# Kernel optimization log

Measured on AMD Instinct MI355X. Metric: run time of the kernel, lower is better.

The kernel has to match this reference:

```python
import jax, jax.numpy as jnp
import numpy as np

DIM = 1024
HEADS = 16
HEAD_DIM = DIM // HEADS
HIDDEN = 4096  # mlp_ratio * dim
SCALE = HEAD_DIM ** -0.5
LN_EPS = 1e-5


def softmax_one(x):
    # softmax with +1 in the denominator (after max subtraction), per source
    m = jnp.max(x, axis=-1, keepdims=True)
    e = jnp.exp(x - m)
    return e / (1.0 + jnp.sum(e, axis=-1, keepdims=True))


def layer_norm(x, g, b):
    mu = jnp.mean(x, axis=-1, keepdims=True)
    var = jnp.mean(jnp.square(x - mu), axis=-1, keepdims=True)
    return (x - mu) * jax.lax.rsqrt(var + LN_EPS) * g + b


def setup_inputs() -> dict:
    key = jax.random.key(0)
    ks = jax.random.split(key, 12)
    B, C, N = 2, DIM, 2048
    x = jax.random.normal(ks[0], (B, C, N), dtype=jnp.float32)
    mask = jax.random.randint(ks[1], (B, HEADS, N), 0, 2, dtype=jnp.int32)
    s = 0.02
    return {
        'x': x,
        'mask': mask,
        'qkv_w': jax.random.normal(ks[2], (3 * DIM, DIM), jnp.float32) * s,
        'qkv_b': jnp.zeros((3 * DIM,), jnp.float32),
        'proj_w': jax.random.normal(ks[3], (DIM, DIM), jnp.float32) * s,
        'proj_b': jnp.zeros((DIM,), jnp.float32),
        'fc1_w': jax.random.normal(ks[4], (HIDDEN, DIM), jnp.float32) * s,
        'fc1_b': jnp.zeros((HIDDEN,), jnp.float32),
        'ln_g': jnp.ones((HIDDEN,), jnp.float32),
        'ln_b': jnp.zeros((HIDDEN,), jnp.float32),
        'fc2_w': jax.random.normal(ks[5], (DIM, HIDDEN), jnp.float32) * s,
        'fc2_b': jnp.zeros((DIM,), jnp.float32),
    }


def reference(x, mask, qkv_w, qkv_b, proj_w, proj_b, fc1_w, fc1_b, ln_g, ln_b, fc2_w, fc2_b):
    B, C, N = x.shape
    xt = jnp.swapaxes(x, 1, 2)  # (B, N, C)

    # ----- attention -----
    qkv = xt @ qkv_w.T + qkv_b                      # (B, N, 3C)
    qkv = qkv.reshape(B, N, 3, HEADS, HEAD_DIM)
    qkv = jnp.transpose(qkv, (2, 0, 3, 1, 4))       # (3, B, H, N, Dh)
    q, k, v = qkv[0], qkv[1], qkv[2]
    scores = jnp.einsum('bhnd,bhmd->bhnm', q * SCALE, k)  # (B, H, N, N)
    scores = jnp.where(mask[:, :, :, None] == 0, -1e9, scores)
    attn = softmax_one(scores)
    out = jnp.einsum('bhnm,bhmd->bhnd', attn, v)    # (B, H, N, Dh)
    # faithful to source: permute(0,3,1,2).reshape(B,N,C) -> scrambled merge
    out = jnp.transpose(out, (0, 3, 1, 2)).reshape(B, N, C)
    out = out @ proj_w.T + proj_b

    # faithful residual: attn_out + ls1(attn_out) with ls1 = Identity
    h = out + out                                   # (B, N, C)

    # ----- MLP (timm Mlp: fc1 -> GELU -> LayerNorm -> fc2) -----
    m = h @ fc1_w.T + fc1_b
    m = jax.nn.gelu(m, approximate=False)
    m = layer_norm(m, ln_g, ln_b)
    m = m @ fc2_w.T + fc2_b
    y = h + m                                       # (B, N, C)

    return jnp.swapaxes(y, 1, 2)                    # (B, C, N)
```

## Files before the change

kernel.cpp:

```cpp
#include <hip/hip_runtime.h>
#include <math.h>

#define DIMC   1024
#define NTOK   2048
#define BATCH  2
#define HEADS  16
#define HDIM   64
#define HIDDEN 4096
#define MROWS  (BATCH*NTOK)
#define QSZ    ((size_t)BATCH*HEADS*NTOK*HDIM)
#define QSC    0.18033688f

typedef unsigned short ushort_t;
typedef __attribute__((ext_vector_type(8))) short short8;
typedef __attribute__((ext_vector_type(4))) float f32x4;
typedef __attribute__((ext_vector_type(4))) unsigned short us4;

__device__ __forceinline__ ushort_t f2b(float f) {
  union { float f; unsigned int u; } cv; cv.f = f;
  unsigned int u = cv.u;
  unsigned int r = (u + 0x7fffu + ((u >> 16) & 1u)) >> 16;
  return (ushort_t)r;
}

__device__ __forceinline__ float b2f(ushort_t b) {
  union { unsigned int u; float f; } cv; cv.u = ((unsigned int)b) << 16;
  return cv.f;
}

__device__ __forceinline__ float fexp2(float x) {
#if __has_builtin(__builtin_amdgcn_exp2f)
  return __builtin_amdgcn_exp2f(x);
#else
  return exp2f(x);
#endif
}

__device__ __forceinline__ void gl_lds16(const void* g, void* l) {
  __builtin_amdgcn_global_load_lds(
      (const __attribute__((address_space(1))) void*)g,
      (__attribute__((address_space(3))) void*)l, 16, 0, 0);
}

__global__ __launch_bounds__(256) void k_pre(const float* __restrict__ x,
                                             const float* __restrict__ w0,
                                             const float* __restrict__ w1,
                                             const float* __restrict__ w2,
                                             const float* __restrict__ w3,
                                             ushort_t* __restrict__ xt,
                                             ushort_t* __restrict__ o0,
                                             ushort_t* __restrict__ o1,
                                             ushort_t* __restrict__ o2,
                                             ushort_t* __restrict__ o3) {
  __shared__ float t[32][33];
  int bid = blockIdx.x;
  if (bid < 4096) {
    int b   = bid >> 11;
    int rem = bid & 2047;
    int n0  = (rem & 63) * 32;
    int c0  = (rem >> 6) * 32;
    int tx = threadIdx.x & 31, ty = threadIdx.x >> 5;
#pragma unroll
    for (int l = 0; l < 4; l++)
      t[ty + l * 8][tx] = x[((size_t)(b * DIMC + c0 + ty + l * 8)) * NTOK + n0 + tx];
    __syncthreads();
#pragma unroll
    for (int l = 0; l < 4; l++)
      xt[((size_t)(b * NTOK + n0 + ty + l * 8)) * DIMC + c0 + tx] = f2b(t[tx][ty + l * 8]);
  } else {
    int cb = bid - 4096;
    const float* in; ushort_t* out; int base;
    if (cb < 3072)      { in = w0; out = o0; base = cb; }
    else if (cb < 4096) { in = w1; out = o1; base = cb - 3072; }
    else if (cb < 8192) { in = w2; out = o2; base = cb - 4096; }
    else                { in = w3; out = o3; base = cb - 8192; }
    int i = base * 256 + threadIdx.x;
    float4 v = ((const float4*)in)[i];
    us4 o; o.x = f2b(v.x); o.y = f2b(v.y); o.z = f2b(v.z); o.w = f2b(v.w);
    ((us4*)out)[i] = o;
  }
}

template <int EPI, int NTX8, int KSTRIDE, int KLEN, int XROW>
__global__ __launch_bounds__(256) void k_gemm_bf16(const ushort_t* __restrict__ A,
                                                   const ushort_t* __restrict__ W,
                                                   const float* __restrict__ bias,
                                                   void* __restrict__ outv) {
  __shared__ ushort_t As[2][128 * 32];
  __shared__ ushort_t Bs[2][128 * 32];
  const int tid = threadIdx.x;
  const int lane = tid & 63, wv = tid >> 6;
  const int bid = blockIdx.x, kz = blockIdx.y;
  const int xcd = bid & 7, t = bid >> 3;
  const int row0 = XROW ? (xcd * NTX8 + (t % NTX8)) * 128 : (t / NTX8) * 128;
  const int col0 = XROW ? (t / NTX8) * 128 : (xcd * NTX8 + (t % NTX8)) * 128;
  const int wrow0 = (wv >> 1) * 64, wcol0 = (wv & 1) * 64;
  const int lm = lane & 15, lq = lane >> 4;
  const int srow = wv * 32 + (lane >> 2);
  const int gch = (lane & 3) ^ ((lane >> 3) & 3);
  const int sw8 = (lq ^ ((lm >> 1) & 3)) * 8;

  const ushort_t* Ab = A + (size_t)(row0 + srow) * KSTRIDE + (size_t)kz * KLEN + gch * 8;
  const ushort_t* Wb = W + (size_t)(col0 + srow) * KSTRIDE + (size_t)kz * KLEN + gch * 8;
  const size_t rstep = (size_t)16 * KSTRIDE;

  f32x4 acc[4][4];
#pragma unroll
  for (int i = 0; i < 4; i++)
#pragma unroll
    for (int j = 0; j < 4; j++) acc[i][j] = (f32x4){0.f, 0.f, 0.f, 0.f};

#define STAGE(buf, k0) do {                                      \
    gl_lds16(Ab + (k0),         &As[buf][wv * 1024]);            \
    gl_lds16(Ab + rstep + (k0), &As[buf][wv * 1024 + 512]);      \
    gl_lds16(Wb + (k0),         &Bs[buf][wv * 1024]);            \
    gl_lds16(Wb + rstep + (k0), &Bs[buf][wv * 1024 + 512]);      \
  } while (0)

  auto compute = [&](int buf) {
    short8 af[4], bf[4];
#pragma unroll
    for (int mi = 0; mi < 4; mi++)
      af[mi] = *(const short8*)&As[buf][(wrow0 + mi * 16 + lm) * 32 + sw8];
#pragma unroll
    for (int ni = 0; ni < 4; ni++)
      bf[ni] = *(const short8*)&Bs[buf][(wcol0 + ni * 16 + lm) * 32 + sw8];
#pragma unroll
    for (int mi = 0; mi < 4; mi++)
#pragma unroll
      for (int ni = 0; ni < 4; ni++)
        acc[mi][ni] = __builtin_amdgcn_mfma_f32_16x16x32_bf16(af[mi], bf[ni], acc[mi][ni], 0, 0, 0);
  };

  constexpr int S = KLEN / 32;
  STAGE(0, 0);
#pragma unroll 1
  for (int kk = 0; kk < S; kk++) {
    __syncthreads();
    if (kk + 1 < S) STAGE((kk + 1) & 1, (kk + 1) * 32);
    compute(kk & 1);
  }
#undef STAGE

#pragma unroll
  for (int mi = 0; mi < 4; mi++) {
#pragma unroll
    for (int ni = 0; ni < 4; ni++) {
#pragma unroll
      for (int r = 0; r < 4; r++) {
        const int row = row0 + wrow0 + mi * 16 + lq * 4 + r;
        const int col = col0 + wcol0 + ni * 16 + lm;
        float v = acc[mi][ni][r];
        if (EPI != 4) v += bias[col];
        if (EPI == 0) {
          int which = col >> 10, rem = col & 1023, hh = rem >> 6, d = rem & 63;
          int bb = row >> 11, n = row & 2047;
          size_t bh = (size_t)(bb * HEADS + hh);
          ushort_t* o16 = (ushort_t*)outv;
          if (which == 0)
            o16[(bh * NTOK + n) * HDIM + d] = f2b(v * QSC);
          else if (which == 1)
            o16[QSZ + (bh * NTOK + n) * HDIM + d] = f2b(v);
          else
            o16[2 * QSZ + (bh * HDIM + d) * NTOK + n] = f2b(v);
        } else {
          ((ushort_t*)outv)[(size_t)kz * MROWS * DIMC + (size_t)row * DIMC + col] = f2b(v);
        }
      }
    }
  }
}

template <int EPI, int KSTRIDE, int NCT, int NB8>
__global__ __launch_bounds__(512, 2) void k_gemm256(const ushort_t* __restrict__ A,
                                                    const ushort_t* __restrict__ W,
                                                    const float* __restrict__ bias,
                                                    void* __restrict__ outv) {
  __shared__ ushort_t As[2][256 * 64];
  __shared__ ushort_t Bs[2][256 * 64];
  const int tid = threadIdx.x;
  const int lane = tid & 63, wid = tid >> 6;
  const int wr = wid >> 2, wc = wid & 3;
  const int lm = lane & 15, quad = lane >> 4;
  const int bid = blockIdx.x, kz = blockIdx.y;
  const int lin = (bid & 7) * NB8 + (bid >> 3);
  const int row0 = (lin / NCT) * 256, col0 = (lin % NCT) * 256;
  const int swz = lm & 7;

  const int gch = (tid & 7) ^ ((tid >> 3) & 7);
  const ushort_t* Ab = A + (size_t)(row0 + (tid >> 3)) * KSTRIDE + (size_t)kz * 1024 + gch * 8;
  const ushort_t* Wb = W + (size_t)(col0 + (tid >> 3)) * KSTRIDE + (size_t)kz * 1024 + gch * 8;
  const int dbase = wid * 512;

  auto stA = [&](int buf, int half, int kt) {
    const ushort_t* s = Ab + (size_t)(half * 128) * KSTRIDE + kt * 64;
    gl_lds16(s,                &As[buf][half * 8192 + dbase]);
    gl_lds16(s + 64 * KSTRIDE, &As[buf][half * 8192 + 4096 + dbase]);
  };
  auto stB = [&](int buf, int half, int kt) {
    const ushort_t* s = Wb + (size_t)(half * 128) * KSTRIDE + kt * 64;
    gl_lds16(s,                &Bs[buf][half * 8192 + dbase]);
    gl_lds16(s + 64 * KSTRIDE, &Bs[buf][half * 8192 + 4096 + dbase]);
  };

  f32x4 acc[8][4];
#pragma unroll
  for (int i = 0; i < 8; i++)
#pragma unroll
    for (int j = 0; j < 4; j++) acc[i][j] = (f32x4){0.f, 0.f, 0.f, 0.f};

  short8 af[4][2], bf[4][2];

  auto rdAf = [&](int buf, int mih) {
#pragma unroll
    for (int mi = 0; mi < 4; mi++)
#pragma unroll
      for (int ks = 0; ks < 2; ks++)
        af[mi][ks] = *(const short8*)&As[buf][(wr * 128 + (mih * 4 + mi) * 16 + lm) * 64 +
                                             (((ks * 4 + quad) ^ swz) * 8)];
  };
  auto rdBf = [&](int buf, int nh) {
#pragma unroll
    for (int nn = 0; nn < 2; nn++)
#pragma unroll
      for (int ks = 0; ks < 2; ks++)
        bf[nh * 2 + nn][ks] = *(const short8*)&Bs[buf][(wc * 64 + (nh * 2 + nn) * 16 + lm) * 64 +
                                                       (((ks * 4 + quad) ^ swz) * 8)];
  };
  auto quadMM = [&](int m0, int n0) {
    __builtin_amdgcn_s_setprio(1);
#pragma unroll
    for (int mi = 0; mi < 4; mi++)
#pragma unroll
      for (int ni = 0; ni < 2; ni++)
#pragma unroll
        for (int ks = 0; ks < 2; ks++)
          acc[m0 + mi][n0 + ni] = __builtin_amdgcn_mfma_f32_16x16x32_bf16(
              af[mi][ks], bf[n0 + ni][ks], acc[m0 + mi][n0 + ni], 0, 0, 0);
    __builtin_amdgcn_s_setprio(0);
  };

  constexpr int NT = 16;
  stB(0, 0, 0); stB(0, 1, 0);
  stA(0, 0, 0); stA(0, 1, 0);
  stB(1, 0, 1); stB(1, 1, 1);

#pragma unroll 1
  for (int kt = 0; kt < NT; kt++) {
    const int buf = kt & 1;
    if (kt + 1 < NT) __builtin_amdgcn_s_waitcnt(0x0F74);
    else             __builtin_amdgcn_s_waitcnt(0x0F70);
    __builtin_amdgcn_s_barrier();
    asm volatile("" ::: "memory");

    rdAf(buf, 0);
    rdBf(buf, 0);
    if (kt + 1 < NT) stA(buf ^ 1, 0, kt + 1);
    asm volatile("" ::: "memory");
    __builtin_amdgcn_s_barrier();
    quadMM(0, 0);
    __builtin_amdgcn_s_barrier();
    asm volatile("" ::: "memory");

    rdBf(buf, 1);
    if (kt + 1 < NT) stA(buf ^ 1, 1, kt + 1);
    asm volatile("" ::: "memory");
    __builtin_amdgcn_s_barrier();
    quadMM(0, 2);
    __builtin_amdgcn_s_barrier();
    asm volatile("" ::: "memory");

    rdAf(buf, 1);
    if (kt + 2 < NT) stB(buf, 0, kt + 2);
    asm volatile("" ::: "memory");
    __builtin_amdgcn_s_barrier();
    quadMM(4, 2);
    __builtin_amdgcn_s_barrier();
    asm volatile("" ::: "memory");

    if (kt + 2 < NT) stB(buf, 1, kt + 2);
    asm volatile("" ::: "memory");
    __builtin_amdgcn_s_barrier();
    quadMM(4, 0);
  }

#pragma unroll
  for (int mi = 0; mi < 8; mi++)
#pragma unroll
    for (int ni = 0; ni < 4; ni++)
#pragma unroll
      for (int r = 0; r < 4; r++) {
        const int row = row0 + wr * 128 + mi * 16 + quad * 4 + r;
        const int col = col0 + wc * 64 + ni * 16 + lm;
        if (EPI == 2) {
          ((ushort_t*)outv)[(size_t)row * HIDDEN + col] = f2b(acc[mi][ni][r] + bias[col]);
        } else {
          ((ushort_t*)outv)[(size_t)kz * MROWS * DIMC + (size_t)row * DIMC + col] = f2b(acc[mi][ni][r]);
        }
      }
}

__global__ __launch_bounds__(256) void k_comb_proj(const ushort_t* __restrict__ p0,
                                                   const ushort_t* __restrict__ p1,
                                                   const float* __restrict__ bias,
                                                   ushort_t* __restrict__ hb) {
  int i = blockIdx.x * 256 + threadIdx.x;
  int colb = (i & 255) * 4;
  us4 a = ((const us4*)p0)[i];
  us4 b = ((const us4*)p1)[i];
  us4 o;
  o.x = f2b(2.f * (b2f(a.x) + b2f(b.x) + bias[colb + 0]));
  o.y = f2b(2.f * (b2f(a.y) + b2f(b.y) + bias[colb + 1]));
  o.z = f2b(2.f * (b2f(a.z) + b2f(b.z) + bias[colb + 2]));
  o.w = f2b(2.f * (b2f(a.w) + b2f(b.w) + bias[colb + 3]));
  ((us4*)hb)[i] = o;
}

__global__ __launch_bounds__(256) void k_comb_fc2(const ushort_t* __restrict__ p,
                                                  const ushort_t* __restrict__ hb,
                                                  const float* __restrict__ bias,
                                                  float* __restrict__ out) {
  __shared__ float t[32][33];
  const size_t SL = (size_t)MROWS * DIMC;
  int b  = blockIdx.z;
  int c0 = blockIdx.y * 32, n0 = blockIdx.x * 32;
  int tx = threadIdx.x, ty = threadIdx.y;
#pragma unroll
  for (int l = 0; l < 4; l++) {
    size_t idx = ((size_t)(b * NTOK + n0 + ty + l * 8)) * DIMC + c0 + tx;
    t[ty + l * 8][tx] = b2f(p[idx]) + b2f(p[idx + SL]) + b2f(p[idx + 2 * SL]) +
                        b2f(p[idx + 3 * SL]) + b2f(hb[idx]) + bias[c0 + tx];
  }
  __syncthreads();
#pragma unroll
  for (int l = 0; l < 4; l++)
    out[((size_t)(b * DIMC + c0 + ty + l * 8)) * NTOK + n0 + tx] = t[tx][ty + l * 8];
}

__global__ __launch_bounds__(256) void k_attn_mfma(const ushort_t* __restrict__ qkv,
                                                   const int* __restrict__ mask,
                                                   ushort_t* __restrict__ scram) {
  __shared__ ushort_t Kl[2][64 * 64];
  __shared__ ushort_t Vl[2][64 * 64];
  __shared__ ushort_t Pl[4 * 32 * 72];
  const int tid = threadIdx.x;
  const int lane = tid & 63, w = tid >> 6;
  const int lm = lane & 15, quad = lane >> 4;
  const int bh = blockIdx.y, b = bh >> 4, h = bh & 15;
  const int q0 = blockIdx.x * 128 + w * 32;
  const ushort_t* qg  = qkv + (size_t)bh * NTOK * HDIM;
  const ushort_t* kg  = qkv + QSZ + (size_t)bh * NTOK * HDIM;
  const ushort_t* vTg = qkv + 2 * QSZ + (size_t)bh * HDIM * NTOK;
  ushort_t* Pw = &Pl[w * 32 * 72];

  const short8 ones = {0x3F80, 0x3F80, 0x3F80, 0x3F80, 0x3F80, 0x3F80, 0x3F80, 0x3F80};

  short8 qf[2][2];
#pragma unroll
  for (int qs = 0; qs < 2; qs++)
#pragma unroll
    for (int hf = 0; hf < 2; hf++)
      qf[qs][hf] = *(const short8*)&qg[(size_t)(q0 + qs * 16 + lm) * HDIM + hf * 32 + quad * 8];

  bool mk[2][4];
#pragma unroll
  for (int qs = 0; qs < 2; qs++)
#pragma unroll
    for (int r = 0; r < 4; r++)
      mk[qs][r] = mask[(size_t)bh * NTOK + q0 + qs * 16 + quad * 4 + r] != 0;

  f32x4 O[2][4], La[2];
#pragma unroll
  for (int qs = 0; qs < 2; qs++) {
    La[qs] = (f32x4){0.f, 0.f, 0.f, 0.f};
#pragma unroll
    for (int r = 0; r < 4; r++) O[qs][r] = (f32x4){0.f, 0.f, 0.f, 0.f};
  }

  const int s0 = tid, s1 = tid + 256;
  const int r0 = s0 >> 3, g0 = (s0 & 7) ^ (r0 & 7);
  const int r1 = s1 >> 3, g1 = (s1 & 7) ^ (r1 & 7);

  gl_lds16(kg + (size_t)r0 * HDIM + g0 * 8, &Kl[0][s0 * 8]);
  gl_lds16(kg + (size_t)r1 * HDIM + g1 * 8, &Kl[0][s1 * 8]);
  gl_lds16(vTg + (size_t)r0 * NTOK + g0 * 8, &Vl[0][s0 * 8]);
  gl_lds16(vTg + (size_t)r1 * NTOK + g1 * 8, &Vl[0][s1 * 8]);

  for (int kt = 0; kt < NTOK; kt += 64) {
    const int cur = (kt >> 6) & 1, nxt = cur ^ 1;
    __syncthreads();
    if (kt + 64 < NTOK) {
      gl_lds16(kg + (size_t)(kt + 64 + r0) * HDIM + g0 * 8, &Kl[nxt][s0 * 8]);
      gl_lds16(kg + (size_t)(kt + 64 + r1) * HDIM + g1 * 8, &Kl[nxt][s1 * 8]);
      gl_lds16(vTg + (size_t)r0 * NTOK + kt + 64 + g0 * 8, &Vl[nxt][s0 * 8]);
      gl_lds16(vTg + (size_t)r1 * NTOK + kt + 64 + g1 * 8, &Vl[nxt][s1 * 8]);
    }

    short8 kf[4][2];
#pragma unroll
    for (int ksub = 0; ksub < 4; ksub++)
#pragma unroll
      for (int hf = 0; hf < 2; hf++)
        kf[ksub][hf] = *(const short8*)&Kl[cur][(ksub * 16 + lm) * 64 + ((4 * hf + quad) ^ (lm & 7)) * 8];

#pragma unroll
    for (int qs = 0; qs < 2; qs++) {
      f32x4 S[4];
#pragma unroll
      for (int ksub = 0; ksub < 4; ksub++) {
        S[ksub] = (f32x4){0.f, 0.f, 0.f, 0.f};
        S[ksub] = __builtin_amdgcn_mfma_f32_16x16x32_bf16(qf[qs][0], kf[ksub][0], S[ksub], 0, 0, 0);
        S[ksub] = __builtin_amdgcn_mfma_f32_16x16x32_bf16(qf[qs][1], kf[ksub][1], S[ksub], 0, 0, 0);
      }
#pragma unroll
      for (int r = 0; r < 4; r++) {
        const int prow = qs * 16 + quad * 4 + r;
#pragma unroll
        for (int ksub = 0; ksub < 4; ksub++) {
          float p = mk[qs][r] ? fexp2(S[ksub][r]) : 1.0f;
          Pw[prow * 72 + ksub * 16 + lm] = (ushort_t)(__float_as_uint(p) >> 16);
        }
      }
    }
    __builtin_amdgcn_s_waitcnt(0xC07F);

    short8 vf[4][2];
#pragma unroll
    for (int dsub = 0; dsub < 4; dsub++)
#pragma unroll
      for (int hf = 0; hf < 2; hf++)
        vf[dsub][hf] = *(const short8*)&Vl[cur][(dsub * 16 + lm) * 64 + ((4 * hf + quad) ^ (lm & 7)) * 8];

#pragma unroll
    for (int qs = 0; qs < 2; qs++) {
      short8 pf[2];
#pragma unroll
      for (int hf = 0; hf < 2; hf++)
        pf[hf] = *(const short8*)&Pw[(qs * 16 + lm) * 72 + hf * 32 + quad * 8];
#pragma unroll
      for (int dsub = 0; dsub < 4; dsub++) {
        O[qs][dsub] = __builtin_amdgcn_mfma_f32_16x16x32_bf16(pf[0], vf[dsub][0], O[qs][dsub], 0, 0, 0);
        O[qs][dsub] = __builtin_amdgcn_mfma_f32_16x16x32_bf16(pf[1], vf[dsub][1], O[qs][dsub], 0, 0, 0);
      }
      La[qs] = __builtin_amdgcn_mfma_f32_16x16x32_bf16(pf[0], ones, La[qs], 0, 0, 0);
      La[qs] = __builtin_amdgcn_mfma_f32_16x16x32_bf16(pf[1], ones, La[qs], 0, 0, 0);
    }
  }

#pragma unroll
  for (int qs = 0; qs < 2; qs++)
#pragma unroll
    for (int r = 0; r < 4; r++) {
      int n = q0 + qs * 16 + quad * 4 + r;
      float inv = 1.f / (1.f + La[qs][r]);
      int n1 = n >> 10, nn0 = n & 1023;
#pragma unroll
      for (int dsub = 0; dsub < 4; dsub++) {
        int d = dsub * 16 + lm;
        int np = d * 32 + h * 2 + n1;
        scram[((size_t)(b * NTOK + np)) * DIMC + nn0] = f2b(O[qs][dsub][r] * inv);
      }
    }
}

__global__ __launch_bounds__(256) void k_ln(ushort_t* __restrict__ mid,
                                            const float* __restrict__ g,
                                            const float* __restrict__ bta) {
  const int row = blockIdx.x;
  ushort_t* p = mid + (size_t)row * HIDDEN;
  const int tid = threadIdx.x;
  float lv[16];
  float s = 0.f, s2 = 0.f;
#pragma unroll
  for (int i = 0; i < 4; i++) {
    us4 u = *(const us4*)&p[tid * 4 + i * 1024];
#pragma unroll
    for (int j = 0; j < 4; j++) {
      float xx = b2f((j == 0) ? u.x : (j == 1) ? u.y : (j == 2) ? u.z : u.w);
      xx = 0.5f * xx * (1.f + erff(xx * 0.70710678118654752f));
      lv[i * 4 + j] = xx;
      s += xx;
      s2 += xx * xx;
    }
  }
#pragma unroll
  for (int off = 32; off > 0; off >>= 1) {
    s += __shfl_down(s, off);
    s2 += __shfl_down(s2, off);
  }
  __shared__ float rs[4], rs2[4];
  if ((tid & 63) == 0) { rs[tid >> 6] = s; rs2[tid >> 6] = s2; }
  __syncthreads();
  float ts = rs[0] + rs[1] + rs[2] + rs[3];
  float ts2 = rs2[0] + rs2[1] + rs2[2] + rs2[3];
  float mu = ts * (1.f / HIDDEN);
  float var = ts2 * (1.f / HIDDEN) - mu * mu;
  float rstd = rsqrtf(var + 1e-5f);
#pragma unroll
  for (int i = 0; i < 4; i++) {
    us4 o;
#pragma unroll
    for (int j = 0; j < 4; j++) {
      int f = tid * 4 + i * 1024 + j;
      float y = (lv[i * 4 + j] - mu) * rstd * g[f] + bta[f];
      ushort_t ob = f2b(y);
      if (j == 0) o.x = ob; else if (j == 1) o.y = ob; else if (j == 2) o.z = ob; else o.w = ob;
    }
    *(us4*)&p[tid * 4 + i * 1024] = o;
  }
}

extern "C" void kernel_launch(void* const* d_in, const int* in_sizes, int n_in,
                              void* d_out, int out_size, void* d_ws, size_t ws_size,
                              hipStream_t stream) {
  const float* x      = (const float*)d_in[0];
  const int*   mask   = (const int*)d_in[1];
  const float* qkv_w  = (const float*)d_in[2];
  const float* qkv_b  = (const float*)d_in[3];
  const float* proj_w = (const float*)d_in[4];
  const float* proj_b = (const float*)d_in[5];
  const float* fc1_w  = (const float*)d_in[6];
  const float* fc1_b  = (const float*)d_in[7];
  const float* ln_g   = (const float*)d_in[8];
  const float* ln_b   = (const float*)d_in[9];
  const float* fc2_w  = (const float*)d_in[10];
  const float* fc2_b  = (const float*)d_in[11];

  char* w = (char*)d_ws;
  ushort_t* qkv16  = (ushort_t*)w;           w += 3 * QSZ * 2;
  ushort_t* xtb    = (ushort_t*)w;           w += (size_t)MROWS * DIMC * 2;
  ushort_t* scramb = (ushort_t*)w;           w += (size_t)MROWS * DIMC * 2;
  ushort_t* hb     = (ushort_t*)w;           w += (size_t)MROWS * DIMC * 2;
  ushort_t* mid    = (ushort_t*)w;           w += (size_t)MROWS * HIDDEN * 2;
  ushort_t* wqkvb  = (ushort_t*)w;           w += (size_t)3 * DIMC * DIMC * 2;
  ushort_t* wprojb = (ushort_t*)w;           w += (size_t)DIMC * DIMC * 2;
  ushort_t* wfc1b  = (ushort_t*)w;           w += (size_t)HIDDEN * DIMC * 2;
  ushort_t* wfc2b  = (ushort_t*)w;           w += (size_t)DIMC * HIDDEN * 2;
  ushort_t* pbuf   = (ushort_t*)w;           w += (size_t)4 * MROWS * DIMC * 2;
  ushort_t* pbuf1  = pbuf + (size_t)MROWS * DIMC;

  k_pre<<<dim3(4096 + 12288), 256, 0, stream>>>(x, qkv_w, proj_w, fc1_w, fc2_w,
                                                xtb, wqkvb, wprojb, wfc1b, wfc2b);

  k_gemm_bf16<0, 4, DIMC, DIMC, 1><<<dim3(24 * 32), 256, 0, stream>>>(
      xtb, wqkvb, qkv_b, qkv16);
  k_attn_mfma<<<dim3(NTOK / 128, BATCH * HEADS), 256, 0, stream>>>(
      qkv16, mask, scramb);
  k_gemm_bf16<4, 4, DIMC, 512, 1><<<dim3(8 * 32, 2), 256, 0, stream>>>(
      scramb, wprojb, nullptr, pbuf);
  k_comb_proj<<<dim3(4096), 256, 0, stream>>>(pbuf, pbuf1, proj_b, hb);
  k_gemm256<2, 1024, 16, 32><<<dim3(256), 512, 0, stream>>>(hb, wfc1b, fc1_b, mid);
  k_ln<<<dim3(MROWS), 256, 0, stream>>>(mid, ln_g, ln_b);
  k_gemm256<4, 4096, 4, 8><<<dim3(64, 4), 512, 0, stream>>>(mid, wfc2b, nullptr, pbuf);
  k_comb_fc2<<<dim3(NTOK / 32, DIMC / 32, BATCH), dim3(32, 8), 0, stream>>>(
      pbuf, hb, fc2_b, (float*)d_out);
}
```

Before: 337.0 us.

## Split attention over key dimension into two halves and combine partials

Splits the attention kernel along the key sequence into two halves (blockIdx.z), each writing unnormalized fp32 output and row-sum partials to scratch buffers, then adds a combine kernel that sums them and normalizes into the scrambled bf16 layout. This doubles the grid from 512 to 1024 blocks to improve occupancy across the GPU's CUs. The combine relies on no running max being subtracted, since partial exp sums add directly. It costs extra fp32 partial writes and reads plus one more launch.

Result: slower. 357.8 us (+6.2%).

```diff
diff --git a/kernel.cpp b/kernel.cpp
--- a/kernel.cpp
+++ b/kernel.cpp
@@ -339,7 +339,8 @@
 
 __global__ __launch_bounds__(256) void k_attn_mfma(const ushort_t* __restrict__ qkv,
                                                    const int* __restrict__ mask,
-                                                   ushort_t* __restrict__ scram) {
+                                                   float* __restrict__ opart,
+                                                   float* __restrict__ lapart) {
   __shared__ ushort_t Kl[2][64 * 64];
   __shared__ ushort_t Vl[2][64 * 64];
   __shared__ ushort_t Pl[4 * 32 * 72];
@@ -347,10 +348,11 @@
   const int lane = tid & 63, w = tid >> 6;
   const int lm = lane & 15, quad = lane >> 4;
   const int bh = blockIdx.y, b = bh >> 4, h = bh & 15;
+  const int kz = blockIdx.z;
   const int q0 = blockIdx.x * 128 + w * 32;
   const ushort_t* qg  = qkv + (size_t)bh * NTOK * HDIM;
-  const ushort_t* kg  = qkv + QSZ + (size_t)bh * NTOK * HDIM;
-  const ushort_t* vTg = qkv + 2 * QSZ + (size_t)bh * HDIM * NTOK;
+  const ushort_t* kg  = qkv + QSZ + (size_t)bh * NTOK * HDIM + (size_t)kz * 1024 * HDIM;
+  const ushort_t* vTg = qkv + 2 * QSZ + (size_t)bh * HDIM * NTOK + (size_t)kz * 1024;
   ushort_t* Pw = &Pl[w * 32 * 72];
 
   const short8 ones = {0x3F80, 0x3F80, 0x3F80, 0x3F80, 0x3F80, 0x3F80, 0x3F80, 0x3F80};
@@ -386,10 +388,10 @@
   gl_lds16(vTg + (size_t)r0 * NTOK + g0 * 8, &Vl[0][s0 * 8]);
   gl_lds16(vTg + (size_t)r1 * NTOK + g1 * 8, &Vl[0][s1 * 8]);
 
-  for (int kt = 0; kt < NTOK; kt += 64) {
+  for (int kt = 0; kt < 1024; kt += 64) {
     const int cur = (kt >> 6) & 1, nxt = cur ^ 1;
     __syncthreads();
-    if (kt + 64 < NTOK) {
+    if (kt + 64 < 1024) {
       gl_lds16(kg + (size_t)(kt + 64 + r0) * HDIM + g0 * 8, &Kl[nxt][s0 * 8]);
       gl_lds16(kg + (size_t)(kt + 64 + r1) * HDIM + g1 * 8, &Kl[nxt][s1 * 8]);
       gl_lds16(vTg + (size_t)r0 * NTOK + kt + 64 + g0 * 8, &Vl[nxt][s0 * 8]);
@@ -452,15 +454,36 @@
 #pragma unroll
     for (int r = 0; r < 4; r++) {
       int n = q0 + qs * 16 + quad * 4 + r;
-      float inv = 1.f / (1.f + La[qs][r]);
       int n1 = n >> 10, nn0 = n & 1023;
+      if (lm == 0)
+        lapart[(size_t)kz * 65536 + (size_t)bh * NTOK + n] = La[qs][r];
 #pragma unroll
       for (int dsub = 0; dsub < 4; dsub++) {
         int d = dsub * 16 + lm;
         int np = d * 32 + h * 2 + n1;
-        scram[((size_t)(b * NTOK + np)) * DIMC + nn0] = f2b(O[qs][dsub][r] * inv);
+        opart[((size_t)kz * 4096 + b * NTOK + np) * 1024 + nn0] = O[qs][dsub][r];
       }
     }
+}
+
+__global__ __launch_bounds__(256) void k_comb_attn(const float* __restrict__ op,
+                                                   const float* __restrict__ la,
+                                                   ushort_t* __restrict__ scram) {
+  const int R = blockIdx.x;
+  const int b = R >> 11, np = R & 2047;
+  const int h = (np >> 1) & 15, n1 = np & 1;
+  const int bh = b * 16 + h;
+  const int i = threadIdx.x * 4;
+  float4 oA = *(const float4*)&op[(size_t)R * 1024 + i];
+  float4 oB = *(const float4*)&op[(size_t)(4096 + R) * 1024 + i];
+  float4 lA = *(const float4*)&la[(size_t)bh * NTOK + n1 * 1024 + i];
+  float4 lB = *(const float4*)&la[65536 + (size_t)bh * NTOK + n1 * 1024 + i];
+  us4 o;
+  o.x = f2b((oA.x + oB.x) / (1.f + lA.x + lB.x));
+  o.y = f2b((oA.y + oB.y) / (1.f + lA.y + lB.y));
+  o.z = f2b((oA.z + oB.z) / (1.f + lA.z + lB.z));
+  o.w = f2b((oA.w + oB.w) / (1.f + lA.w + lB.w));
+  *(us4*)&scram[(size_t)R * 1024 + i] = o;
 }
 
 __global__ __launch_bounds__(256) void k_ln(ushort_t* __restrict__ mid,
@@ -538,14 +561,17 @@
   ushort_t* wfc2b  = (ushort_t*)w;           w += (size_t)DIMC * HIDDEN * 2;
   ushort_t* pbuf   = (ushort_t*)w;           w += (size_t)4 * MROWS * DIMC * 2;
   ushort_t* pbuf1  = pbuf + (size_t)MROWS * DIMC;
+  float* opart  = (float*)pbuf;
+  float* lapart = (float*)mid;
 
   k_pre<<<dim3(4096 + 12288), 256, 0, stream>>>(x, qkv_w, proj_w, fc1_w, fc2_w,
                                                 xtb, wqkvb, wprojb, wfc1b, wfc2b);
 
   k_gemm_bf16<0, 4, DIMC, DIMC, 1><<<dim3(24 * 32), 256, 0, stream>>>(
       xtb, wqkvb, qkv_b, qkv16);
-  k_attn_mfma<<<dim3(NTOK / 128, BATCH * HEADS), 256, 0, stream>>>(
-      qkv16, mask, scramb);
+  k_attn_mfma<<<dim3(NTOK / 128, BATCH * HEADS, 2), 256, 0, stream>>>(
+      qkv16, mask, opart, lapart);
+  k_comb_attn<<<dim3(4096), 256, 0, stream>>>(opart, lapart, scramb);
   k_gemm_bf16<4, 4, DIMC, 512, 1><<<dim3(8 * 32, 2), 256, 0, stream>>>(
       scramb, wprojb, nullptr, pbuf);
   k_comb_proj<<<dim3(4096), 256, 0, stream>>>(pbuf, pbuf1, proj_b, hb);
```
